# Optimization experiments

Hardware: AMD Instinct MI355X
Metric: run time of the kernel (lower is better)

Reference implementation:

```python
import jax, jax.numpy as jnp
import numpy as np

N = 100_000   # nodes
E = 1_600_000 # message-passing edges
EA = 1_000_000 # aux edges for bilinear head
G = 512       # graphs in batch
F_IN = 16     # num_node_features (fixed in source)
H = 32        # hidden_dim (fixed in source)


def setup_inputs() -> dict:
    key = jax.random.key(0)
    ks = jax.random.split(key, 8)
    x = jax.random.normal(ks[0], (N, F_IN), jnp.float32)
    edge_index = jax.random.randint(ks[1], (2, E), 0, N, dtype=jnp.int32)
    edge_index_aux = jax.random.randint(ks[2], (2, EA), 0, N, dtype=jnp.int32)
    batch = jnp.sort(jax.random.randint(ks[3], (N,), 0, G, dtype=jnp.int32))
    W1 = jax.random.normal(ks[4], (F_IN, H), jnp.float32) / np.sqrt(F_IN)
    b1 = jnp.zeros((H,), jnp.float32)
    W2 = jax.random.normal(ks[5], (H, H), jnp.float32) / np.sqrt(H)
    b2 = jnp.zeros((H,), jnp.float32)
    Wr = jax.random.normal(ks[6], (H, 1), jnp.float32) / np.sqrt(H)
    br = jnp.zeros((1,), jnp.float32)
    Wbil = jax.random.normal(ks[7], (1, H, H), jnp.float32) / H
    bbil = jnp.zeros((1,), jnp.float32)
    return dict(x=x, edge_index=edge_index, edge_index_aux=edge_index_aux,
                batch=batch, W1=W1, b1=b1, W2=W2, b2=b2, Wr=Wr, br=br,
                Wbil=Wbil, bbil=bbil)


def gcn_conv(x, W, b, src, dst):
    # PyG GCNConv: x' = D^{-1/2}(A+I)D^{-1/2} (x W) + b, deg includes self-loop
    xw = x @ W                                                   # [N,H]
    deg = jax.ops.segment_sum(jnp.ones((src.shape[0],), x.dtype), dst,
                              num_segments=N) + 1.0              # +1 self-loop
    dinv = jax.lax.rsqrt(deg)                                    # [N]
    coef = dinv[src] * dinv[dst]                                 # [E]
    agg = jax.ops.segment_sum(xw[src] * coef[:, None], dst, num_segments=N)
    agg = agg + xw * (dinv * dinv)[:, None]                      # self-loop msg
    return agg + b


def reference(x, edge_index, edge_index_aux, batch,
              W1, b1, W2, b2, Wr, br, Wbil, bbil):
    src, dst = edge_index[0], edge_index[1]
    h = jax.nn.relu(gcn_conv(x, W1, b1, src, dst))
    h = gcn_conv(h, W2, b2, src, dst)
    # global_mean_pool over graph ids
    cnt = jax.ops.segment_sum(jnp.ones((N,), h.dtype), batch, num_segments=G)
    pooled = jax.ops.segment_sum(h, batch, num_segments=G) / jnp.maximum(cnt, 1.0)[:, None]
    reg_output = pooled @ Wr + br                                # [G,1]
    # Bilinear edge head: out_e = x1_e^T W x2_e + b
    h1 = h[edge_index_aux[0]]                                    # [EA,H]
    h2 = h[edge_index_aux[1]]                                    # [EA,H]
    edge_pred = jnp.einsum('ei,ij,ej->e', h1, Wbil[0], h2)[:, None] + bbil
    return reg_output, edge_pred
```

## Files before the change

### kernel.cpp

```cpp
#include <hip/hip_runtime.h>
#include <hip/hip_bf16.h>
#include <string.h>

typedef __hip_bfloat16 bf16;

#define FIN 16
#define H   32
#define PADW 64
#define NB  512
#define BINCAP 4096
#define NPBMAX 200
#define PSTRIDE 65
#define CHUNK 8192
#define SCAN_CHUNK 1024
#define MAXSEG 64

__device__ __forceinline__ float b2f(bf16 v) { return __bfloat162float(v); }

__device__ __forceinline__ float loadf(const void* p, size_t i, int f32) {
    return f32 ? ((const float*)p)[i] : b2f(((const bf16*)p)[i]);
}
__device__ __forceinline__ void storef(void* p, size_t i, float v, int f32) {
    if (f32) ((float*)p)[i] = v;
    else     ((bf16*)p)[i] = __float2bfloat16(v);
}

__device__ __forceinline__ unsigned pack2(float lo, float hi) {
    bf16 a = __float2bfloat16(lo), b = __float2bfloat16(hi);
    unsigned short ua, ub;
    memcpy(&ua, &a, 2); memcpy(&ub, &b, 2);
    return ((unsigned)ub << 16) | (unsigned)ua;
}
__device__ __forceinline__ float f_lo(unsigned u) {
    union { unsigned i; float f; } v; v.i = u << 16; return v.f;
}
__device__ __forceinline__ float f_hi(unsigned u) {
    union { unsigned i; float f; } v; v.i = u & 0xffff0000u; return v.f;
}

__global__ void k_detect(const void* __restrict__ x, int nelem, int* __restrict__ flag) {
    __shared__ int cnt;
    if (threadIdx.x == 0) cnt = 0;
    __syncthreads();
    int bad = 0;
    const bf16* p = (const bf16*)x;
    for (int i = threadIdx.x; i < nelem; i += blockDim.x) {
        float v = b2f(p[i]);
        float a = fabsf(v);
        if (isnan(v) || a > 1024.f || (v != 0.f && a < 1e-20f)) bad++;
    }
    atomicAdd(&cnt, bad);
    __syncthreads();
    if (threadIdx.x == 0) flag[0] = (cnt > 64) ? 1 : 0;
}

__global__ void __launch_bounds__(1024) k_p1(
        const int* __restrict__ src, const int* __restrict__ dst,
        int* __restrict__ bincur, unsigned* __restrict__ binbuf,
        int E, int npb) {
    __shared__ int hcnt[4][NB];
    __shared__ int hbase[NB];
    __shared__ int scur[NB];
    int tid = threadIdx.x;
    int grp = tid >> 8;
    int e0 = blockIdx.x * CHUNK;
    int nE = E - e0;
    if (nE > CHUNK) nE = CHUNK;
    for (int i = tid; i < 4 * NB; i += blockDim.x) ((int*)hcnt)[i] = 0;
    __syncthreads();
    for (int i = tid; i < nE; i += blockDim.x)
        atomicAdd(&hcnt[grp][dst[e0 + i] / npb], 1);
    __syncthreads();
    for (int i = tid; i < NB; i += blockDim.x) {
        int c = hcnt[0][i] + hcnt[1][i] + hcnt[2][i] + hcnt[3][i];
        hbase[i] = c ? atomicAdd(&bincur[i], c) : 0;
        scur[i] = 0;
    }
    __syncthreads();
    for (int i = tid; i < nE; i += blockDim.x) {
        int d = dst[e0 + i];
        int bin = d / npb;
        int pos = hbase[bin] + atomicAdd(&scur[bin], 1);
        if (pos < BINCAP)
            binbuf[(size_t)bin * BINCAP + pos] =
                ((unsigned)src[e0 + i] << 10) | (unsigned)(d - bin * npb);
    }
}

__global__ void __launch_bounds__(256) k_p2(
        const int* __restrict__ bincur, const unsigned* __restrict__ binbuf,
        int* __restrict__ csr, int* __restrict__ deg, float* __restrict__ dinv,
        int N, int npb) {
    __shared__ int cur[NPBMAX];
    __shared__ int psr[NPBMAX * PSTRIDE];
    int b = blockIdx.x;
    int base = b * npb;
    int nn = N - base;
    if (nn > npb) nn = npb;
    if (nn < 0) nn = 0;
    for (int i = threadIdx.x; i < nn; i += blockDim.x) cur[i] = 0;
    __syncthreads();
    int cnt = bincur[b];
    if (cnt > BINCAP) cnt = BINCAP;
    const unsigned* buf = binbuf + (size_t)b * BINCAP;
    for (int j = threadIdx.x; j < cnt; j += blockDim.x) {
        unsigned p = buf[j];
        int loc = (int)(p & 1023u);
        int s = (int)(p >> 10);
        int pos = atomicAdd(&cur[loc], 1);
        if (pos < PADW) psr[loc * PSTRIDE + pos] = s;
    }
    __syncthreads();
    int tot = nn * PADW;
    for (int idx = threadIdx.x; idx < tot; idx += blockDim.x) {
        int i = idx >> 6, p = idx & 63;
        csr[((size_t)(base + i) << 6) + p] = psr[i * PSTRIDE + p];
    }
    for (int i = threadIdx.x; i < nn; i += blockDim.x) {
        int dg = cur[i];
        deg[base + i] = dg;
        dinv[base + i] = rsqrtf((float)dg + 1.0f);
    }
}


__global__ void k_fillp(const int* __restrict__ src, const int* __restrict__ dst,
                        int* __restrict__ cursor, int* __restrict__ csr, int E) {
    int e = blockIdx.x * blockDim.x + threadIdx.x;
    if (e >= E) return;
    int d = dst[e];
    int pos = atomicAdd(&cursor[d], 1);
    if (pos < PADW) csr[((size_t)d << 6) + pos] = src[e];
}

__global__ void k_dinvi(const int* __restrict__ deg, float* __restrict__ dinv, int N) {
    int t = blockIdx.x * blockDim.x + threadIdx.x;
    if (t < N) dinv[t] = rsqrtf((float)deg[t] + 1.0f);
}

__global__ void k_gatherpb(const int* __restrict__ deg, const int* __restrict__ csr,
                           const float* __restrict__ dinv, const unsigned* __restrict__ xsb,
                           float2* __restrict__ agg, int N) {
    int t = blockIdx.x * blockDim.x + threadIdx.x;
    int d = t >> 4, j = t & 15;
    if (d >= N) return;
    int len = deg[d];
    if (len > PADW) len = PADW;
    const int* lst = csr + ((size_t)d << 6);
    unsigned u = xsb[(size_t)d * 16 + j];
    float a0 = f_lo(u), a1 = f_hi(u);
    float b0 = 0.f, b1 = 0.f;
    int k = 0;
    for (; k + 1 < len; k += 2) {
        int s0 = lst[k], s1 = lst[k + 1];
        unsigned u0 = xsb[(size_t)s0 * 16 + j];
        unsigned u1 = xsb[(size_t)s1 * 16 + j];
        a0 += f_lo(u0); a1 += f_hi(u0);
        b0 += f_lo(u1); b1 += f_hi(u1);
    }
    if (k < len) {
        unsigned u2 = xsb[(size_t)lst[k] * 16 + j];
        a0 += f_lo(u2); a1 += f_hi(u2);
    }
    float dv = dinv[d];
    agg[(size_t)d * 16 + j] = make_float2((a0 + b0) * dv, (a1 + b1) * dv);
}


__global__ void __launch_bounds__(256) k_xw1v(
        const void* __restrict__ x, const void* __restrict__ W1,
        const float* __restrict__ dinv, const int* __restrict__ flag,
        unsigned* __restrict__ xsb, int N) {
    __shared__ float sW[FIN * H];
    __shared__ float sxx[16 * 17];
    int f32 = flag[0];
    for (int i = threadIdx.x; i < FIN * H; i += blockDim.x) sW[i] = loadf(W1, i, f32);
    __syncthreads();
    int t = blockIdx.x * blockDim.x + threadIdx.x;
    int n = t >> 4, j = t & 15, g = threadIdx.x >> 4;
    if (n < N) sxx[g * 17 + j] = loadf(x, (size_t)n * FIN + j, f32);
    __syncthreads();
    if (n >= N) return;
    float dv = dinv[n];
    float s0 = 0.f, s1 = 0.f;
    const float* xp = &sxx[g * 17];
#pragma unroll
    for (int i = 0; i < FIN; i++) {
        float xv = xp[i];
        s0 += xv * sW[i * H + 2 * j];
        s1 += xv * sW[i * H + 2 * j + 1];
    }
    xsb[(size_t)n * 16 + j] = pack2(s0 * dv, s1 * dv);
}

__global__ void __launch_bounds__(256) k_h1xw2v(
        const void* __restrict__ W2, const void* __restrict__ b1,
        const float* __restrict__ dinv, const int* __restrict__ flag,
        const float2* __restrict__ aggv, unsigned* __restrict__ xsb2, int N) {
    __shared__ float sW[H * H];
    __shared__ float sb[H];
    __shared__ float shh[16 * 33];
    int f32 = flag[0];
    for (int i = threadIdx.x; i < H * H; i += blockDim.x) sW[i] = loadf(W2, i, f32);
    if (threadIdx.x < H) sb[threadIdx.x] = loadf(b1, threadIdx.x, f32);
    __syncthreads();
    int t = blockIdx.x * blockDim.x + threadIdx.x;
    int n = t >> 4, j = t & 15, g = threadIdx.x >> 4;
    if (n < N) {
        float2 a = aggv[(size_t)n * 16 + j];
        float v0 = a.x + sb[2 * j], v1 = a.y + sb[2 * j + 1];
        shh[g * 33 + 2 * j]     = v0 > 0.f ? v0 : 0.f;
        shh[g * 33 + 2 * j + 1] = v1 > 0.f ? v1 : 0.f;
    }
    __syncthreads();
    if (n >= N) return;
    float dv = dinv[n];
    float s0 = 0.f, s1 = 0.f;
    const float* hp = &shh[g * 33];
#pragma unroll
    for (int i = 0; i < H; i++) {
        float hv = hp[i];
        s0 += hv * sW[i * H + 2 * j];
        s1 += hv * sW[i * H + 2 * j + 1];
    }
    xsb2[(size_t)n * 16 + j] = pack2(s0 * dv, s1 * dv);
}

__global__ void __launch_bounds__(256) k_hb(
        const void* __restrict__ b2v, const void* __restrict__ Wbil,
        const int* __restrict__ flag, const float2* __restrict__ aggv,
        unsigned* __restrict__ hb32, unsigned* __restrict__ gb32, int N) {
    __shared__ float sW[H * H];
    __shared__ float sb[H];
    __shared__ float shh[16 * 33];
    int f32 = flag[0];
    for (int i = threadIdx.x; i < H * H; i += blockDim.x) sW[i] = loadf(Wbil, i, f32);
    if (threadIdx.x < H) sb[threadIdx.x] = loadf(b2v, threadIdx.x, f32);
    __syncthreads();
    int t = blockIdx.x * blockDim.x + threadIdx.x;
    int n = t >> 4, j = t & 15, g = threadIdx.x >> 4;
    if (n < N) {
        float2 a = aggv[(size_t)n * 16 + j];
        float v0 = a.x + sb[2 * j], v1 = a.y + sb[2 * j + 1];
        shh[g * 33 + 2 * j]     = v0;
        shh[g * 33 + 2 * j + 1] = v1;
        hb32[(size_t)n * 16 + j] = pack2(v0, v1);
    }
    __syncthreads();
    if (n >= N) return;
    float s0 = 0.f, s1 = 0.f;
    const float* hp = &shh[g * 33];
#pragma unroll
    for (int i = 0; i < H; i++) {
        float hv = hp[i];
        s0 += hv * sW[i * H + 2 * j];
        s1 += hv * sW[i * H + 2 * j + 1];
    }
    gb32[(size_t)n * 16 + j] = pack2(s0, s1);
}

__global__ void __launch_bounds__(256) k_pool(
        const void* __restrict__ b2v, const int* __restrict__ batch,
        const int* __restrict__ flag, const float* __restrict__ aggB,
        float* __restrict__ pooled, float* __restrict__ cnt, int N) {
    __shared__ float sb[H];
    __shared__ int   sg[256];
    __shared__ float spool[MAXSEG * H];
    __shared__ float scnt[MAXSEG];
    int f32 = flag[0];
    if (threadIdx.x < H) sb[threadIdx.x] = loadf(b2v, threadIdx.x, f32);
    int blk0 = blockIdx.x * blockDim.x;
    int nvalid = N - blk0;
    if (nvalid > (int)blockDim.x) nvalid = blockDim.x;
    if ((int)threadIdx.x < nvalid) sg[threadIdx.x] = batch[blk0 + threadIdx.x];
    __syncthreads();
    int g0 = sg[0];
    int nseg = sg[nvalid - 1] - g0 + 1;
    int f = threadIdx.x & 31, k = threadIdx.x >> 5;
    if (nseg <= MAXSEG) {
        for (int i = threadIdx.x; i < nseg * H; i += blockDim.x) spool[i] = 0.f;
        for (int i = threadIdx.x; i < nseg; i += blockDim.x) scnt[i] = 0.f;
        __syncthreads();
        for (int r = k; r < nvalid; r += 8) {
            float v = aggB[(size_t)(blk0 + r) * H + f] + sb[f];
            int gl = sg[r] - g0;
            atomicAdd(&spool[gl * H + f], v);
            if (f == 0) atomicAdd(&scnt[gl], 1.f);
        }
        __syncthreads();
        for (int i = threadIdx.x; i < nseg * H; i += blockDim.x)
            atomicAdd(&pooled[(size_t)(g0 + (i >> 5)) * H + (i & 31)], spool[i]);
        for (int i = threadIdx.x; i < nseg; i += blockDim.x)
            atomicAdd(&cnt[g0 + i], scnt[i]);
    } else {
        for (int r = k; r < nvalid; r += 8) {
            float v = aggB[(size_t)(blk0 + r) * H + f] + sb[f];
            atomicAdd(&pooled[(size_t)sg[r] * H + f], v);
            if (f == 0) atomicAdd(&cnt[sg[r]], 1.f);
        }
    }
}


__global__ void k_degi(const int* __restrict__ dst, int* __restrict__ deg, int E) {
    int t = blockIdx.x * blockDim.x + threadIdx.x;
    if (t < E) atomicAdd(&deg[dst[t]], 1);
}

__global__ void k_scan1(const int* __restrict__ deg, int* __restrict__ partials, int N) {
    __shared__ int sd[256];
    int base = blockIdx.x * SCAN_CHUNK + threadIdx.x * 4;
    int s = 0;
#pragma unroll
    for (int k = 0; k < 4; k++) { int i = base + k; s += (i < N) ? deg[i] : 0; }
    sd[threadIdx.x] = s;
    __syncthreads();
    for (int off = 128; off > 0; off >>= 1) {
        if (threadIdx.x < off) sd[threadIdx.x] += sd[threadIdx.x + off];
        __syncthreads();
    }
    if (threadIdx.x == 0) partials[blockIdx.x] = sd[0];
}

__global__ void k_scan2(const int* __restrict__ partials, int* __restrict__ chunk_off, int B1) {
    __shared__ int sd[256];
    int t = threadIdx.x;
    int lv[4];
    int s = 0;
#pragma unroll
    for (int k = 0; k < 4; k++) { int i = t * 4 + k; lv[k] = (i < B1) ? partials[i] : 0; s += lv[k]; }
    sd[t] = s;
    __syncthreads();
    int inc = s;
    for (int off = 1; off < 256; off <<= 1) {
        int v = (t >= off) ? sd[t - off] : 0;
        __syncthreads();
        sd[t] += v;
        __syncthreads();
    }
    int run = sd[t] - inc;
#pragma unroll
    for (int k = 0; k < 4; k++) { int i = t * 4 + k; if (i < B1) chunk_off[i] = run; run += lv[k]; }
    if (t == 255) chunk_off[B1] = run;
}

__global__ void k_scan3(const int* __restrict__ deg, const int* __restrict__ chunk_off,
                        int* __restrict__ row_ptr, int* __restrict__ cursor,
                        int N, int E) {
    __shared__ int sd[256];
    int t = threadIdx.x;
    int base = blockIdx.x * SCAN_CHUNK + t * 4;
    int lv[4];
    int s = 0;
#pragma unroll
    for (int k = 0; k < 4; k++) { int i = base + k; lv[k] = (i < N) ? deg[i] : 0; s += lv[k]; }
    sd[t] = s;
    __syncthreads();
    int inc = s;
    for (int off = 1; off < 256; off <<= 1) {
        int v = (t >= off) ? sd[t - off] : 0;
        __syncthreads();
        sd[t] += v;
        __syncthreads();
    }
    int run = chunk_off[blockIdx.x] + sd[t] - inc;
#pragma unroll
    for (int k = 0; k < 4; k++) {
        int i = base + k;
        if (i < N) { row_ptr[i] = run; cursor[i] = run; }
        run += lv[k];
    }
    if (blockIdx.x == 0 && t == 0) row_ptr[N] = E;
}

__global__ void k_fill(const int* __restrict__ src, const int* __restrict__ dst,
                       int* __restrict__ cursor, int* __restrict__ csr, int E) {
    int e = blockIdx.x * blockDim.x + threadIdx.x;
    if (e >= E) return;
    int pos = atomicAdd(&cursor[dst[e]], 1);
    csr[pos] = src[e];
}

__global__ void k_gather(const int* __restrict__ row_ptr, const int* __restrict__ csr,
                         const float* __restrict__ dinv, const float* __restrict__ xs,
                         float* __restrict__ agg, int N) {
    int t = blockIdx.x * blockDim.x + threadIdx.x;
    int d = t >> 5, f = t & 31;
    if (d >= N) return;
    int beg = row_ptr[d], end = row_ptr[d + 1];
    float acc  = xs[(size_t)d * H + f];
    float acc2 = 0.f;
    int j = beg;
    for (; j + 1 < end; j += 2) {
        int s0 = csr[j], s1 = csr[j + 1];
        acc  += xs[(size_t)s0 * H + f];
        acc2 += xs[(size_t)s1 * H + f];
    }
    if (j < end) acc += xs[(size_t)csr[j] * H + f];
    agg[(size_t)d * H + f] = (acc + acc2) * dinv[d];
}

__global__ void k_xw1n(const void* __restrict__ x, const void* __restrict__ W1,
                       const float* __restrict__ dinv, const int* __restrict__ flag,
                       float* __restrict__ xs, int N) {
    __shared__ float sW[FIN * H];
    int f32 = flag[0];
    for (int i = threadIdx.x; i < FIN * H; i += blockDim.x) sW[i] = loadf(W1, i, f32);
    __syncthreads();
    int n = blockIdx.x * blockDim.x + threadIdx.x;
    if (n >= N) return;
    float xr[FIN];
#pragma unroll
    for (int i = 0; i < FIN; i++) xr[i] = loadf(x, (size_t)n * FIN + i, f32);
    float dv = dinv[n];
#pragma unroll
    for (int f = 0; f < H; f++) {
        float s = 0.f;
#pragma unroll
        for (int i = 0; i < FIN; i++) s += xr[i] * sW[i * H + f];
        xs[(size_t)n * H + f] = s * dv;
    }
}

__global__ void k_h1xw2n(const void* __restrict__ W2, const void* __restrict__ b1,
                         const float* __restrict__ dinv, const int* __restrict__ flag,
                         const float* __restrict__ agg, float* __restrict__ xs2, int N) {
    __shared__ float sW[H * H];
    __shared__ float sb[H];
    int f32 = flag[0];
    for (int i = threadIdx.x; i < H * H; i += blockDim.x) sW[i] = loadf(W2, i, f32);
    if (threadIdx.x < H) sb[threadIdx.x] = loadf(b1, threadIdx.x, f32);
    __syncthreads();
    int n = blockIdx.x * blockDim.x + threadIdx.x;
    if (n >= N) return;
    float hr[H];
#pragma unroll
    for (int f = 0; f < H; f++) {
        float v = agg[(size_t)n * H + f] + sb[f];
        hr[f] = v > 0.f ? v : 0.f;
    }
    float dv = dinv[n];
#pragma unroll
    for (int f = 0; f < H; f++) {
        float s = 0.f;
#pragma unroll
        for (int i = 0; i < H; i++) s += hr[i] * sW[i * H + f];
        xs2[(size_t)n * H + f] = s * dv;
    }
}


__global__ void k_degf(const int* __restrict__ dst, float* __restrict__ deg, int E) {
    int t = blockIdx.x * blockDim.x + threadIdx.x;
    if (t < E) atomicAdd(&deg[dst[t]], 1.0f);
}
__global__ void k_dinvf(float* __restrict__ deg, int N) {
    int t = blockIdx.x * blockDim.x + threadIdx.x;
    if (t < N) deg[t] = rsqrtf(deg[t] + 1.0f);
}
__global__ void k_xw1o(const void* __restrict__ x, const void* __restrict__ W1,
                       const float* __restrict__ dinv, const int* __restrict__ flag,
                       float* __restrict__ xw, float* __restrict__ agg, int N) {
    __shared__ float sW[FIN * H];
    int f32 = flag[0];
    for (int i = threadIdx.x; i < FIN * H; i += blockDim.x) sW[i] = loadf(W1, i, f32);
    __syncthreads();
    int n = blockIdx.x * blockDim.x + threadIdx.x;
    if (n >= N) return;
    float xr[FIN];
#pragma unroll
    for (int i = 0; i < FIN; i++) xr[i] = loadf(x, (size_t)n * FIN + i, f32);
    float dv = dinv[n], dv2 = dv * dv;
#pragma unroll
    for (int f = 0; f < H; f++) {
        float s = 0.f;
#pragma unroll
        for (int i = 0; i < FIN; i++) s += xr[i] * sW[i * H + f];
        xw[(size_t)n * H + f]  = s;
        agg[(size_t)n * H + f] = s * dv2;
    }
}
__global__ void k_scatter(const int* __restrict__ src, const int* __restrict__ dst,
                          const float* __restrict__ dinv, const float* __restrict__ xw,
                          float* __restrict__ agg, int E) {
    int t = blockIdx.x * blockDim.x + threadIdx.x;
    int e = t >> 5, f = t & 31;
    if (e >= E) return;
    int s = src[e], d = dst[e];
    float c = dinv[s] * dinv[d];
    atomicAdd(&agg[(size_t)d * H + f], xw[(size_t)s * H + f] * c);
}
__global__ void k_h1xw2o(const void* __restrict__ W2, const void* __restrict__ b1,
                         const float* __restrict__ dinv, const int* __restrict__ flag,
                         float* __restrict__ aggio, float* __restrict__ xw2, int N) {
    __shared__ float sW[H * H];
    __shared__ float sb[H];
    int f32 = flag[0];
    for (int i = threadIdx.x; i < H * H; i += blockDim.x) sW[i] = loadf(W2, i, f32);
    if (threadIdx.x < H) sb[threadIdx.x] = loadf(b1, threadIdx.x, f32);
    __syncthreads();
    int n = blockIdx.x * blockDim.x + threadIdx.x;
    if (n >= N) return;
    float hr[H];
#pragma unroll
    for (int f = 0; f < H; f++) {
        float v = aggio[(size_t)n * H + f] + sb[f];
        hr[f] = v > 0.f ? v : 0.f;
    }
    float dv = dinv[n], dv2 = dv * dv;
#pragma unroll
    for (int f = 0; f < H; f++) {
        float s = 0.f;
#pragma unroll
        for (int i = 0; i < H; i++) s += hr[i] * sW[i * H + f];
        xw2[(size_t)n * H + f]   = s;
        aggio[(size_t)n * H + f] = s * dv2;
    }
}


__global__ void k_reg(const float* __restrict__ pooled, const float* __restrict__ cnt,
                      const void* __restrict__ Wr, const void* __restrict__ br,
                      const int* __restrict__ flag, void* __restrict__ out, int G) {
    int f32 = flag[0];
    int g = blockIdx.x * blockDim.x + threadIdx.x;
    if (g >= G) return;
    float c = cnt[g];
    c = c > 1.f ? c : 1.f;
    float s = 0.f;
#pragma unroll
    for (int i = 0; i < H; i++) s += pooled[(size_t)g * H + i] * loadf(Wr, i, f32);
    storef(out, g, s / c + loadf(br, 0, f32), f32);
}

__global__ void k_bil(const int* __restrict__ srcA, const int* __restrict__ dstA,
                      const unsigned* __restrict__ gb32, const unsigned* __restrict__ hb32,
                      const void* __restrict__ bbil, const int* __restrict__ flag,
                      void* __restrict__ out, int G, int EA) {
    int f32 = flag[0];
    int e = blockIdx.x * blockDim.x + threadIdx.x;
    if (e >= EA) return;
    int s = srcA[e], d = dstA[e];
    const uint4* gp = (const uint4*)(gb32 + (size_t)s * (H / 2));
    const uint4* hp = (const uint4*)(hb32 + (size_t)d * (H / 2));
    float acc = 0.f;
#pragma unroll
    for (int k = 0; k < 4; k++) {
        uint4 a = gp[k], b = hp[k];
        acc += f_lo(a.x) * f_lo(b.x) + f_hi(a.x) * f_hi(b.x);
        acc += f_lo(a.y) * f_lo(b.y) + f_hi(a.y) * f_hi(b.y);
        acc += f_lo(a.z) * f_lo(b.z) + f_hi(a.z) * f_hi(b.z);
        acc += f_lo(a.w) * f_lo(b.w) + f_hi(a.w) * f_hi(b.w);
    }
    storef(out, (size_t)G + e, acc + loadf(bbil, 0, f32), f32);
}

extern "C" void kernel_launch(void* const* d_in, const int* in_sizes, int n_in,
                              void* d_out, int out_size, void* d_ws, size_t ws_size,
                              hipStream_t stream) {
    const void* x     = d_in[0];
    const int*  ei    = (const int*)d_in[1];
    const int*  eia   = (const int*)d_in[2];
    const int*  batch = (const int*)d_in[3];
    const void* W1    = d_in[4];
    const void* b1    = d_in[5];
    const void* W2    = d_in[6];
    const void* b2    = d_in[7];
    const void* Wr    = d_in[8];
    const void* br    = d_in[9];
    const void* Wbil  = d_in[10];
    const void* bbil  = d_in[11];

    const int N  = in_sizes[0] / FIN;
    const int E  = in_sizes[1] / 2;
    const int EA = in_sizes[2] / 2;
    const int G  = out_size - EA;

    float* ws     = (float*)d_ws;
    int*   flag   = (int*)ws;
    float* dinv   = ws + 16;
    float* A      = dinv + N;
    float* B      = A + (size_t)N * H;
    float* pooled = B + (size_t)N * H;
    float* cnt    = pooled + (size_t)G * H;
    float* fend   = cnt + G;

    unsigned* xsb  = (unsigned*)A;
    unsigned* hb32 = (unsigned*)A;
    unsigned* gb32 = hb32 + (size_t)N * (H / 2);

    int* degA   = (int*)fend;
    int* csrA   = degA + N;
    int* bincur = csrA + (size_t)N * PADW;
    size_t needA  = (size_t)((char*)bincur - (char*)d_ws);
    size_t needA2 = (size_t)((char*)(bincur + NB) - (char*)d_ws);
    const int B1 = (N + SCAN_CHUNK - 1) / SCAN_CHUNK;
    int* deg_i     = (int*)fend;
    int* curB      = deg_i + N;
    int* row_ptr   = curB + N;
    int* chunk_off = row_ptr + N + 1;
    int* csrB      = chunk_off + B1 + 1;
    size_t needB = (size_t)((char*)(csrB + E) - (char*)d_ws);

    const int npb = (N + NB - 1) / NB;
    const bool tierA2 = (ws_size >= needA2) && (npb <= NPBMAX) && (N <= (1 << 22)) &&
                        ((size_t)NB * BINCAP <= (size_t)N * H * 2);
    const bool tierA  = !tierA2 && (ws_size >= needA);
    const bool tierB  = !tierA2 && !tierA && (ws_size >= needB) && (B1 <= 1024);

    const int* src  = ei;
    const int* dst  = ei + E;
    const int* srcA = eia;
    const int* dstA = eia + EA;

    const int TB = 256;
    hipMemsetAsync(pooled, 0, ((size_t)G * H + G) * sizeof(float), stream);
    k_detect<<<1, TB, 0, stream>>>(x, 1024, flag);

    int ggrid16 = (int)(((long)N * 16 + TB - 1) / TB);
    int ggrid32 = (int)(((long)N * 32 + TB - 1) / TB);
    int ngrid   = (N + TB - 1) / TB;
    unsigned* xsb2 = xsb;
    float2* aggv = (float2*)B;

    if (tierA2) {
        unsigned* binbuf = (unsigned*)A;
        hipMemsetAsync(bincur, 0, NB * sizeof(int), stream);
        int nblk1 = (E + CHUNK - 1) / CHUNK;
        k_p1<<<nblk1, 1024, 0, stream>>>(src, dst, bincur, binbuf, E, npb);
        k_p2<<<NB, TB, 0, stream>>>(bincur, binbuf, csrA, degA, dinv, N, npb);
        k_xw1v<<<ggrid16, TB, 0, stream>>>(x, W1, dinv, flag, xsb, N);
        k_gatherpb<<<ggrid16, TB, 0, stream>>>(degA, csrA, dinv, xsb, aggv, N);
        k_h1xw2v<<<ggrid16, TB, 0, stream>>>(W2, b1, dinv, flag, aggv, xsb2, N);
        k_gatherpb<<<ggrid16, TB, 0, stream>>>(degA, csrA, dinv, xsb2, aggv, N);
    } else if (tierA) {
        hipMemsetAsync(degA, 0, (size_t)N * sizeof(int), stream);
        k_fillp<<<(E + TB - 1) / TB, TB, 0, stream>>>(src, dst, degA, csrA, E);
        k_dinvi<<<ngrid, TB, 0, stream>>>(degA, dinv, N);
        k_xw1v<<<ggrid16, TB, 0, stream>>>(x, W1, dinv, flag, xsb, N);
        k_gatherpb<<<ggrid16, TB, 0, stream>>>(degA, csrA, dinv, xsb, aggv, N);
        k_h1xw2v<<<ggrid16, TB, 0, stream>>>(W2, b1, dinv, flag, aggv, xsb2, N);
        k_gatherpb<<<ggrid16, TB, 0, stream>>>(degA, csrA, dinv, xsb2, aggv, N);
    } else if (tierB) {
        hipMemsetAsync(deg_i, 0, (size_t)N * sizeof(int), stream);
        k_degi<<<(E + TB - 1) / TB, TB, 0, stream>>>(dst, deg_i, E);
        k_dinvi<<<ngrid, TB, 0, stream>>>(deg_i, dinv, N);
        k_scan1<<<B1, TB, 0, stream>>>(deg_i, chunk_off, N);
        k_scan2<<<1, TB, 0, stream>>>(chunk_off, chunk_off, B1);
        k_scan3<<<B1, TB, 0, stream>>>(deg_i, chunk_off, row_ptr, curB, N, E);
        k_fill<<<(E + TB - 1) / TB, TB, 0, stream>>>(src, dst, curB, csrB, E);
        k_xw1n<<<ngrid, TB, 0, stream>>>(x, W1, dinv, flag, A, N);
        k_gather<<<ggrid32, TB, 0, stream>>>(row_ptr, csrB, dinv, A, B, N);
        k_h1xw2n<<<ngrid, TB, 0, stream>>>(W2, b1, dinv, flag, B, A, N);
        k_gather<<<ggrid32, TB, 0, stream>>>(row_ptr, csrB, dinv, A, B, N);
    } else {
        hipMemsetAsync(dinv, 0, (size_t)N * sizeof(float), stream);
        k_degf<<<(E + TB - 1) / TB, TB, 0, stream>>>(dst, dinv, E);
        k_dinvf<<<ngrid, TB, 0, stream>>>(dinv, N);
        k_xw1o<<<ngrid, TB, 0, stream>>>(x, W1, dinv, flag, A, B, N);
        long tot = (long)E * 32;
        int sgrid = (int)((tot + TB - 1) / TB);
        k_scatter<<<sgrid, TB, 0, stream>>>(src, dst, dinv, A, B, E);
        k_h1xw2o<<<ngrid, TB, 0, stream>>>(W2, b1, dinv, flag, B, A, N);
        k_scatter<<<sgrid, TB, 0, stream>>>(src, dst, dinv, A, B, E);
    }

    k_pool<<<ngrid, TB, 0, stream>>>(b2, batch, flag, B, pooled, cnt, N);
    k_hb<<<ggrid16, TB, 0, stream>>>(b2, Wbil, flag, aggv, hb32, gb32, N);
    k_reg<<<(G + TB - 1) / TB, TB, 0, stream>>>(pooled, cnt, Wr, br, flag, d_out, G);
    k_bil<<<(EA + TB - 1) / TB, TB, 0, stream>>>(srcA, dstA, gb32, hb32, bbil, flag, d_out, G, EA);
}
```

Measured before the change: 290.9 us.

## Fuse pooling with bilinear prep, fuse edge head with regression, trim launches

Merges the mean-pool kernel and the bilinear-projection kernel into one 512-thread kernel that computes the biased h once, keeps it in shared memory, and feeds both pooling and the Wbil product. It also merges the regression and bilinear edge-head kernels into one launch. The two memsets move into the detect kernel, and the CSR build now writes only the valid slots instead of full 64-entry padded rows. The gather loop is unrolled by four using int4 index loads, which needs an aligned CSR base, so the CSR pointer is now aligned to 16 bytes. The aim is fewer launches, fewer memory passes over h, and more memory-level parallelism, at the cost of higher shared-memory use per block in the fused pool kernel.

```diff
diff --git a/kernel.cpp b/kernel.cpp
--- a/kernel.cpp
+++ b/kernel.cpp
@@ -1,6 +1,7 @@
 #include <hip/hip_runtime.h>
 #include <hip/hip_bf16.h>
 #include <string.h>
+#include <stdint.h>
 
 typedef __hip_bfloat16 bf16;
 
@@ -14,6 +15,7 @@
 #define CHUNK 8192
 #define SCAN_CHUNK 1024
 #define MAXSEG 64
+#define POOLBLK 256
 
 __device__ __forceinline__ float b2f(bf16 v) { return __bfloat162float(v); }
 
@@ -38,9 +40,13 @@
     union { unsigned i; float f; } v; v.i = u & 0xffff0000u; return v.f;
 }
 
-__global__ void k_detect(const void* __restrict__ x, int nelem, int* __restrict__ flag) {
-    __shared__ int cnt;
-    if (threadIdx.x == 0) cnt = 0;
+__global__ void k_detect(const void* __restrict__ x, int nelem, int* __restrict__ flag,
+                         float* __restrict__ zf, int nzf,
+                         int* __restrict__ zi, int nzi) {
+    for (int i = threadIdx.x; i < nzf; i += blockDim.x) zf[i] = 0.f;
+    if (zi) for (int i = threadIdx.x; i < nzi; i += blockDim.x) zi[i] = 0;
+    __shared__ int cntS;
+    if (threadIdx.x == 0) cntS = 0;
     __syncthreads();
     int bad = 0;
     const bf16* p = (const bf16*)x;
@@ -49,9 +55,9 @@
         float a = fabsf(v);
         if (isnan(v) || a > 1024.f || (v != 0.f && a < 1e-20f)) bad++;
     }
-    atomicAdd(&cnt, bad);
-    __syncthreads();
-    if (threadIdx.x == 0) flag[0] = (cnt > 64) ? 1 : 0;
+    atomicAdd(&cntS, bad);
+    __syncthreads();
+    if (threadIdx.x == 0) flag[0] = (cntS > 64) ? 1 : 0;
 }
 
 __global__ void __launch_bounds__(1024) k_p1(
@@ -114,7 +120,10 @@
     int tot = nn * PADW;
     for (int idx = threadIdx.x; idx < tot; idx += blockDim.x) {
         int i = idx >> 6, p = idx & 63;
-        csr[((size_t)(base + i) << 6) + p] = psr[i * PSTRIDE + p];
+        int dg = cur[i];
+        if (dg > PADW) dg = PADW;
+        if (p < dg)
+            csr[((size_t)(base + i) << 6) + p] = psr[i * PSTRIDE + p];
     }
     for (int i = threadIdx.x; i < nn; i += blockDim.x) {
         int dg = cur[i];
@@ -151,14 +160,18 @@
     float a0 = f_lo(u), a1 = f_hi(u);
     float b0 = 0.f, b1 = 0.f;
     int k = 0;
-    for (; k + 1 < len; k += 2) {
-        int s0 = lst[k], s1 = lst[k + 1];
-        unsigned u0 = xsb[(size_t)s0 * 16 + j];
-        unsigned u1 = xsb[(size_t)s1 * 16 + j];
+    for (; k + 4 <= len; k += 4) {
+        int4 s4 = *(const int4*)(lst + k);
+        unsigned u0 = xsb[(size_t)s4.x * 16 + j];
+        unsigned u1 = xsb[(size_t)s4.y * 16 + j];
+        unsigned u2 = xsb[(size_t)s4.z * 16 + j];
+        unsigned u3 = xsb[(size_t)s4.w * 16 + j];
         a0 += f_lo(u0); a1 += f_hi(u0);
         b0 += f_lo(u1); b1 += f_hi(u1);
-    }
-    if (k < len) {
+        a0 += f_lo(u2); a1 += f_hi(u2);
+        b0 += f_lo(u3); b1 += f_hi(u3);
+    }
+    for (; k < len; k++) {
         unsigned u2 = xsb[(size_t)lst[k] * 16 + j];
         a0 += f_lo(u2); a1 += f_hi(u2);
     }
@@ -226,78 +239,62 @@
     xsb2[(size_t)n * 16 + j] = pack2(s0 * dv, s1 * dv);
 }
 
-__global__ void __launch_bounds__(256) k_hb(
+__global__ void __launch_bounds__(512) k_poolhb(
         const void* __restrict__ b2v, const void* __restrict__ Wbil,
-        const int* __restrict__ flag, const float2* __restrict__ aggv,
-        unsigned* __restrict__ hb32, unsigned* __restrict__ gb32, int N) {
+        const int* __restrict__ batch, const int* __restrict__ flag,
+        const float* __restrict__ aggB, float* __restrict__ pooled,
+        float* __restrict__ cnt, bf16* __restrict__ hb, bf16* __restrict__ gb,
+        int N) {
     __shared__ float sW[H * H];
     __shared__ float sb[H];
-    __shared__ float shh[16 * 33];
-    int f32 = flag[0];
-    for (int i = threadIdx.x; i < H * H; i += blockDim.x) sW[i] = loadf(Wbil, i, f32);
-    if (threadIdx.x < H) sb[threadIdx.x] = loadf(b2v, threadIdx.x, f32);
-    __syncthreads();
-    int t = blockIdx.x * blockDim.x + threadIdx.x;
-    int n = t >> 4, j = t & 15, g = threadIdx.x >> 4;
-    if (n < N) {
-        float2 a = aggv[(size_t)n * 16 + j];
-        float v0 = a.x + sb[2 * j], v1 = a.y + sb[2 * j + 1];
-        shh[g * 33 + 2 * j]     = v0;
-        shh[g * 33 + 2 * j + 1] = v1;
-        hb32[(size_t)n * 16 + j] = pack2(v0, v1);
-    }
-    __syncthreads();
-    if (n >= N) return;
-    float s0 = 0.f, s1 = 0.f;
-    const float* hp = &shh[g * 33];
-#pragma unroll
-    for (int i = 0; i < H; i++) {
-        float hv = hp[i];
-        s0 += hv * sW[i * H + 2 * j];
-        s1 += hv * sW[i * H + 2 * j + 1];
-    }
-    gb32[(size_t)n * 16 + j] = pack2(s0, s1);
-}
-
-__global__ void __launch_bounds__(256) k_pool(
-        const void* __restrict__ b2v, const int* __restrict__ batch,
-        const int* __restrict__ flag, const float* __restrict__ aggB,
-        float* __restrict__ pooled, float* __restrict__ cnt, int N) {
-    __shared__ float sb[H];
-    __shared__ int   sg[256];
+    __shared__ float sh[POOLBLK][H];
+    __shared__ int   sg[POOLBLK];
     __shared__ float spool[MAXSEG * H];
     __shared__ float scnt[MAXSEG];
     int f32 = flag[0];
-    if (threadIdx.x < H) sb[threadIdx.x] = loadf(b2v, threadIdx.x, f32);
-    int blk0 = blockIdx.x * blockDim.x;
+    int tid = threadIdx.x;
+    for (int i = tid; i < H * H; i += blockDim.x) sW[i] = loadf(Wbil, i, f32);
+    if (tid < H) sb[tid] = loadf(b2v, tid, f32);
+    int blk0 = blockIdx.x * POOLBLK;
     int nvalid = N - blk0;
-    if (nvalid > (int)blockDim.x) nvalid = blockDim.x;
-    if ((int)threadIdx.x < nvalid) sg[threadIdx.x] = batch[blk0 + threadIdx.x];
+    if (nvalid > POOLBLK) nvalid = POOLBLK;
+    if (tid < nvalid) sg[tid] = batch[blk0 + tid];
+    for (int i = tid; i < MAXSEG * H; i += blockDim.x) spool[i] = 0.f;
+    if (tid < MAXSEG) scnt[tid] = 0.f;
+    __syncthreads();
+    int f = tid & 31, k = tid >> 5;
+    for (int r = k; r < nvalid; r += 16) {
+        float v = aggB[(size_t)(blk0 + r) * H + f] + sb[f];
+        sh[r][f] = v;
+        hb[(size_t)(blk0 + r) * H + f] = __float2bfloat16(v);
+    }
     __syncthreads();
     int g0 = sg[0];
     int nseg = sg[nvalid - 1] - g0 + 1;
-    int f = threadIdx.x & 31, k = threadIdx.x >> 5;
     if (nseg <= MAXSEG) {
-        for (int i = threadIdx.x; i < nseg * H; i += blockDim.x) spool[i] = 0.f;
-        for (int i = threadIdx.x; i < nseg; i += blockDim.x) scnt[i] = 0.f;
-        __syncthreads();
-        for (int r = k; r < nvalid; r += 8) {
-            float v = aggB[(size_t)(blk0 + r) * H + f] + sb[f];
+        for (int r = k; r < nvalid; r += 16) {
             int gl = sg[r] - g0;
-            atomicAdd(&spool[gl * H + f], v);
+            atomicAdd(&spool[gl * H + f], sh[r][f]);
             if (f == 0) atomicAdd(&scnt[gl], 1.f);
         }
-        __syncthreads();
-        for (int i = threadIdx.x; i < nseg * H; i += blockDim.x)
-            atomicAdd(&pooled[(size_t)(g0 + (i >> 5)) * H + (i & 31)], spool[i]);
-        for (int i = threadIdx.x; i < nseg; i += blockDim.x)
-            atomicAdd(&cnt[g0 + i], scnt[i]);
     } else {
-        for (int r = k; r < nvalid; r += 8) {
-            float v = aggB[(size_t)(blk0 + r) * H + f] + sb[f];
-            atomicAdd(&pooled[(size_t)sg[r] * H + f], v);
+        for (int r = k; r < nvalid; r += 16) {
+            atomicAdd(&pooled[(size_t)sg[r] * H + f], sh[r][f]);
             if (f == 0) atomicAdd(&cnt[sg[r]], 1.f);
         }
+    }
+    for (int r = k; r < nvalid; r += 16) {
+        float s = 0.f;
+#pragma unroll
+        for (int i = 0; i < H; i++) s += sh[r][i] * sW[i * H + f];
+        gb[(size_t)(blk0 + r) * H + f] = __float2bfloat16(s);
+    }
+    if (nseg <= MAXSEG) {
+        __syncthreads();
+        for (int i = tid; i < nseg * H; i += blockDim.x)
+            atomicAdd(&pooled[(size_t)(g0 + (i >> 5)) * H + (i & 31)], spool[i]);
+        for (int i = tid; i < nseg; i += blockDim.x)
+            atomicAdd(&cnt[g0 + i], scnt[i]);
     }
 }
 
@@ -519,40 +516,40 @@
 }
 
 
-__global__ void k_reg(const float* __restrict__ pooled, const float* __restrict__ cnt,
-                      const void* __restrict__ Wr, const void* __restrict__ br,
-                      const int* __restrict__ flag, void* __restrict__ out, int G) {
-    int f32 = flag[0];
-    int g = blockIdx.x * blockDim.x + threadIdx.x;
-    if (g >= G) return;
-    float c = cnt[g];
-    c = c > 1.f ? c : 1.f;
-    float s = 0.f;
-#pragma unroll
-    for (int i = 0; i < H; i++) s += pooled[(size_t)g * H + i] * loadf(Wr, i, f32);
-    storef(out, g, s / c + loadf(br, 0, f32), f32);
-}
-
-__global__ void k_bil(const int* __restrict__ srcA, const int* __restrict__ dstA,
-                      const unsigned* __restrict__ gb32, const unsigned* __restrict__ hb32,
-                      const void* __restrict__ bbil, const int* __restrict__ flag,
-                      void* __restrict__ out, int G, int EA) {
-    int f32 = flag[0];
-    int e = blockIdx.x * blockDim.x + threadIdx.x;
-    if (e >= EA) return;
-    int s = srcA[e], d = dstA[e];
-    const uint4* gp = (const uint4*)(gb32 + (size_t)s * (H / 2));
-    const uint4* hp = (const uint4*)(hb32 + (size_t)d * (H / 2));
-    float acc = 0.f;
-#pragma unroll
-    for (int k = 0; k < 4; k++) {
-        uint4 a = gp[k], b = hp[k];
-        acc += f_lo(a.x) * f_lo(b.x) + f_hi(a.x) * f_hi(b.x);
-        acc += f_lo(a.y) * f_lo(b.y) + f_hi(a.y) * f_hi(b.y);
-        acc += f_lo(a.z) * f_lo(b.z) + f_hi(a.z) * f_hi(b.z);
-        acc += f_lo(a.w) * f_lo(b.w) + f_hi(a.w) * f_hi(b.w);
-    }
-    storef(out, (size_t)G + e, acc + loadf(bbil, 0, f32), f32);
+__global__ void k_bilreg(const int* __restrict__ srcA, const int* __restrict__ dstA,
+                         const unsigned* __restrict__ gb32, const unsigned* __restrict__ hb32,
+                         const void* __restrict__ bbil,
+                         const float* __restrict__ pooled, const float* __restrict__ cnt,
+                         const void* __restrict__ Wr, const void* __restrict__ br,
+                         const int* __restrict__ flag, void* __restrict__ out,
+                         int G, int EA) {
+    int f32 = flag[0];
+    int t = blockIdx.x * blockDim.x + threadIdx.x;
+    if (t < EA) {
+        int s = srcA[t], d = dstA[t];
+        const uint4* gp = (const uint4*)(gb32 + (size_t)s * (H / 2));
+        const uint4* hp = (const uint4*)(hb32 + (size_t)d * (H / 2));
+        float acc = 0.f;
+#pragma unroll
+        for (int kk = 0; kk < 4; kk++) {
+            uint4 a = gp[kk], b = hp[kk];
+            acc += f_lo(a.x) * f_lo(b.x) + f_hi(a.x) * f_hi(b.x);
+            acc += f_lo(a.y) * f_lo(b.y) + f_hi(a.y) * f_hi(b.y);
+            acc += f_lo(a.z) * f_lo(b.z) + f_hi(a.z) * f_hi(b.z);
+            acc += f_lo(a.w) * f_lo(b.w) + f_hi(a.w) * f_hi(b.w);
+        }
+        storef(out, (size_t)G + t, acc + loadf(bbil, 0, f32), f32);
+    } else {
+        int g = t - EA;
+        if (g < G) {
+            float c = cnt[g];
+            c = c > 1.f ? c : 1.f;
+            float s = 0.f;
+#pragma unroll
+            for (int i = 0; i < H; i++) s += pooled[(size_t)g * H + i] * loadf(Wr, i, f32);
+            storef(out, g, s / c + loadf(br, 0, f32), f32);
+        }
+    }
 }
 
 extern "C" void kernel_launch(void* const* d_in, const int* in_sizes, int n_in,
@@ -590,7 +587,7 @@
     unsigned* gb32 = hb32 + (size_t)N * (H / 2);
 
     int* degA   = (int*)fend;
-    int* csrA   = degA + N;
+    int* csrA   = (int*)(((uintptr_t)(degA + N) + 15) & ~(uintptr_t)15);
     int* bincur = csrA + (size_t)N * PADW;
     size_t needA  = (size_t)((char*)bincur - (char*)d_ws);
     size_t needA2 = (size_t)((char*)(bincur + NB) - (char*)d_ws);
@@ -614,8 +611,11 @@
     const int* dstA = eia + EA;
 
     const int TB = 256;
-    hipMemsetAsync(pooled, 0, ((size_t)G * H + G) * sizeof(float), stream);
-    k_detect<<<1, TB, 0, stream>>>(x, 1024, flag);
+    const int npool = G * H + G;
+
+    k_detect<<<1, 1024, 0, stream>>>(x, 1024, flag, pooled, npool,
+                                     tierA2 ? bincur : (int*)nullptr,
+                                     tierA2 ? NB : 0);
 
     int ggrid16 = (int)(((long)N * 16 + TB - 1) / TB);
     int ggrid32 = (int)(((long)N * 32 + TB - 1) / TB);
@@ -625,7 +625,6 @@
 
     if (tierA2) {
         unsigned* binbuf = (unsigned*)A;
-        hipMemsetAsync(bincur, 0, NB * sizeof(int), stream);
         int nblk1 = (E + CHUNK - 1) / CHUNK;
         k_p1<<<nblk1, 1024, 0, stream>>>(src, dst, bincur, binbuf, E, npb);
         k_p2<<<NB, TB, 0, stream>>>(bincur, binbuf, csrA, degA, dinv, N, npb);
@@ -665,8 +664,8 @@
         k_scatter<<<sgrid, TB, 0, stream>>>(src, dst, dinv, A, B, E);
     }
 
-    k_pool<<<ngrid, TB, 0, stream>>>(b2, batch, flag, B, pooled, cnt, N);
-    k_hb<<<ggrid16, TB, 0, stream>>>(b2, Wbil, flag, aggv, hb32, gb32, N);
-    k_reg<<<(G + TB - 1) / TB, TB, 0, stream>>>(pooled, cnt, Wr, br, flag, d_out, G);
-    k_bil<<<(EA + TB - 1) / TB, TB, 0, stream>>>(srcA, dstA, gb32, hb32, bbil, flag, d_out, G, EA);
-}
+    k_poolhb<<<(N + POOLBLK - 1) / POOLBLK, 512, 0, stream>>>(
+        b2, Wbil, batch, flag, B, pooled, cnt, (bf16*)hb32, (bf16*)gb32, N);
+    k_bilreg<<<(EA + G + TB - 1) / TB, TB, 0, stream>>>(
+        srcA, dstA, gb32, hb32, bbil, pooled, cnt, Wr, br, flag, d_out, G, EA);
+}
```

Result: faster. 274.4 us (-5.7%).
